# Optimization experiments

Measured on AMD Instinct MI355X. Metric: run time of the kernel, lower is better.

## Reference

```python
import jax, jax.numpy as jnp
import numpy as np

TEMPERATURE = 0.5
EPS = 1e-8  # torch F.cosine_similarity norm clamp


def setup_inputs() -> dict:
    key = jax.random.key(0)
    k1, k2 = jax.random.split(key)
    N, D = 4096, 256
    z1 = jax.random.normal(k1, (N, D), dtype=jnp.float32)
    z2 = jax.random.normal(k2, (N, D), dtype=jnp.float32)
    return {"z1": z1, "z2": z2}


def _l2norm(x):
    # matches torch cosine_similarity eps clamping on the norm
    n = jnp.sqrt(jnp.sum(x * x, axis=-1, keepdims=True))
    return x / jnp.maximum(n, EPS)


def reference(z1, z2):
    N = z1.shape[0]
    f = jnp.concatenate([z1, z2], axis=0)          # [2N, D]
    fn = _l2norm(f)                                 # row-normalized
    sim = fn @ fn.T                                 # [2N, 2N] cosine similarities
    diag = jnp.eye(2 * N, dtype=bool)
    # denominator: sum over off-diagonal entries (self-similarity excluded)
    denom = jnp.sum(jnp.where(diag, 0.0, jnp.exp(sim / TEMPERATURE)), axis=1)  # [2N]
    # positives: cosine(z1_i, z2_i), duplicated for both views
    z1n, z2n = _l2norm(z1), _l2norm(z2)
    pos = jnp.sum(z1n * z2n, axis=1)               # [N]
    pos = jnp.concatenate([pos, pos], axis=0)      # [2N]
    loss = -jnp.mean(jnp.log(jnp.exp(pos / TEMPERATURE) / denom))
    return loss
```

## Files before the change

### kernel.cpp

```cpp
#include <hip/hip_runtime.h>
#include <hip/hip_fp8.h>

#define D 256
#define SCALE 1.69864354f
#define EPS 1e-8f

typedef __attribute__((ext_vector_type(4))) float f32x4;
typedef long fp8x8;

__global__ __launch_bounds__(256) void normpos_kernel(
    const float* __restrict__ z1, const float* __restrict__ z2,
    unsigned char* __restrict__ fnq, float* __restrict__ pos,
    int* __restrict__ sync, int N) {
  if (blockIdx.x == 0 && threadIdx.x == 0) *sync = 0;
  int wid  = threadIdx.x >> 6;
  int lane = threadIdx.x & 63;
  int row  = blockIdx.x * 4 + wid;
  f32x4 a = *(const f32x4*)(z1 + (size_t)row * D + lane * 4);
  f32x4 b = *(const f32x4*)(z2 + (size_t)row * D + lane * 4);
  float s1  = a.x * a.x + a.y * a.y + a.z * a.z + a.w * a.w;
  float s2  = b.x * b.x + b.y * b.y + b.z * b.z + b.w * b.w;
  float dot = a.x * b.x + a.y * b.y + a.z * b.z + a.w * b.w;
  #pragma unroll
  for (int m = 1; m < 64; m <<= 1) {
    s1  += __shfl_xor(s1, m, 64);
    s2  += __shfl_xor(s2, m, 64);
    dot += __shfl_xor(dot, m, 64);
  }
  float inv1 = 1.0f / fmaxf(sqrtf(s1), EPS);
  float inv2 = 1.0f / fmaxf(sqrtf(s2), EPS);
  float q1 = inv1 * SCALE, q2 = inv2 * SCALE;
  unsigned int w1 = 0, w2 = 0;
  #pragma unroll
  for (int j = 0; j < 4; ++j) {
    w1 |= (unsigned int)__hip_cvt_float_to_fp8(a[j] * q1, __HIP_SATFINITE,
                                               __HIP_E4M3) << (8 * j);
    w2 |= (unsigned int)__hip_cvt_float_to_fp8(b[j] * q2, __HIP_SATFINITE,
                                               __HIP_E4M3) << (8 * j);
  }
  *(unsigned int*)(fnq + (size_t)row * D + lane * 4)       = w1;
  *(unsigned int*)(fnq + (size_t)(N + row) * D + lane * 4) = w2;
  if (lane == 0) pos[row] = dot * inv1 * inv2;
}


__device__ __forceinline__ void stage_tile(const unsigned char* __restrict__ row0,
                                           int kk, unsigned char* lds, int tid) {
  #pragma unroll
  for (int it = 0; it < 4; ++it) {
    int s = it * 256 + tid;
    int r = s >> 3;
    int p = s & 7;
    const unsigned char* src =
        row0 + (size_t)r * D + kk * 128 + ((p ^ (r & 7)) << 4);
    __builtin_amdgcn_global_load_lds(
        (const __attribute__((address_space(1))) void*)src,
        (__attribute__((address_space(3))) void*)(lds + s * 16), 16, 0, 0);
  }
}

__global__ __launch_bounds__(256, 4) void denom_kernel(
    const unsigned char* __restrict__ fnq, float* __restrict__ partial,
    int twoN) {
  __shared__ unsigned char As[128 * 128];
  __shared__ unsigned char Bs[128 * 128];

  int tid  = threadIdx.x;
  int wid  = tid >> 6;
  int lane = tid & 63;
  int c = lane & 15;
  int g = lane >> 4;
  int wr = wid >> 1, wc = wid & 1;

  int bid = blockIdx.x;
  int i = (int)((sqrtf(8.f * (float)bid + 1.f) - 1.f) * 0.5f);
  while ((i + 1) * (i + 2) / 2 <= bid) ++i;
  while (i * (i + 1) / 2 > bid) --i;
  int rb = bid - i * (i + 1) / 2;
  int cb = i;
  const unsigned char* Arow0 = fnq + (size_t)rb * 128 * D;
  const unsigned char* Brow0 = fnq + (size_t)cb * 128 * D;

  bool dblk  = (rb == cb);
  bool dwave = dblk && (wr == wc);

  f32x4 acc[4][4] = {};

  stage_tile(Arow0, 0, As, tid);
  stage_tile(Brow0, 0, Bs, tid);

  #pragma unroll
  for (int kk = 0; kk < 2; ++kk) {
    __syncthreads();
    #pragma unroll
    for (int ks = 0; ks < 4; ++ks) {
      fp8x8 a[4], b[4];
      int q  = (ks << 1) | (g >> 1);
      int h  = (g & 1) << 3;
      #pragma unroll
      for (int mi = 0; mi < 4; ++mi) {
        int ar = wr * 64 + mi * 16 + c;
        a[mi] = *(const fp8x8*)(As + ar * 128 + ((q ^ (ar & 7)) << 4) + h);
      }
      #pragma unroll
      for (int ni = 0; ni < 4; ++ni) {
        int bc = wc * 64 + ni * 16 + c;
        b[ni] = *(const fp8x8*)(Bs + bc * 128 + ((q ^ (bc & 7)) << 4) + h);
      }
      #pragma unroll
      for (int mi = 0; mi < 4; ++mi)
        #pragma unroll
        for (int ni = 0; ni < 4; ++ni)
          acc[mi][ni] = __builtin_amdgcn_mfma_f32_16x16x32_fp8_fp8(
              a[mi], b[ni], acc[mi][ni], 0, 0, 0);
    }
    if (kk == 0) {
      __syncthreads();
      stage_tile(Arow0, 1, As, tid);
      stage_tile(Brow0, 1, Bs, tid);
    }
  }

  float rsum[16];
  float csum[4];
  #pragma unroll
  for (int ii = 0; ii < 16; ++ii) rsum[ii] = 0.f;
  #pragma unroll
  for (int ii = 0; ii < 4; ++ii) csum[ii] = 0.f;

  if (dwave) {
    #pragma unroll
    for (int mi = 0; mi < 4; ++mi)
      #pragma unroll
      for (int ni = 0; ni < 4; ++ni) {
        int colloc = ni * 16 + c;
        #pragma unroll
        for (int r = 0; r < 4; ++r) {
          int rowloc = mi * 16 + g * 4 + r;
          float e = __builtin_amdgcn_exp2f(acc[mi][ni][r]);
          if (rowloc == colloc) e = 0.f;
          rsum[mi * 4 + r] += e;
        }
      }
  } else if (dblk) {
    #pragma unroll
    for (int mi = 0; mi < 4; ++mi)
      #pragma unroll
      for (int ni = 0; ni < 4; ++ni)
        #pragma unroll
        for (int r = 0; r < 4; ++r)
          rsum[mi * 4 + r] += __builtin_amdgcn_exp2f(acc[mi][ni][r]);
  } else {
    #pragma unroll
    for (int mi = 0; mi < 4; ++mi)
      #pragma unroll
      for (int ni = 0; ni < 4; ++ni)
        #pragma unroll
        for (int r = 0; r < 4; ++r) {
          float e = __builtin_amdgcn_exp2f(acc[mi][ni][r]);
          rsum[mi * 4 + r] += e;
          csum[ni]         += e;
        }
  }

  #pragma unroll
  for (int ii = 0; ii < 16; ++ii) {
    float v = rsum[ii];
    v += __shfl_xor(v, 1, 64);
    v += __shfl_xor(v, 2, 64);
    v += __shfl_xor(v, 4, 64);
    v += __shfl_xor(v, 8, 64);
    rsum[ii] = v;
  }
  if (!dblk) {
    #pragma unroll
    for (int ii = 0; ii < 4; ++ii) {
      float v = csum[ii];
      v += __shfl_xor(v, 16, 64);
      v += __shfl_xor(v, 32, 64);
      csum[ii] = v;
    }
  }

  __syncthreads();
  float* redR = (float*)As;
  float* redC = (float*)Bs;
  if (c == 0) {
    #pragma unroll
    for (int mi = 0; mi < 4; ++mi)
      #pragma unroll
      for (int r = 0; r < 4; ++r)
        redR[(wr * 64 + mi * 16 + g * 4 + r) * 2 + wc] = rsum[mi * 4 + r];
  }
  if (!dblk && g == 0) {
    #pragma unroll
    for (int ni = 0; ni < 4; ++ni)
      redC[(wc * 64 + ni * 16 + c) * 2 + wr] = csum[ni];
  }
  __syncthreads();
  if (tid < 128) {
    partial[(size_t)cb * twoN + rb * 128 + tid] =
        redR[tid * 2] + redR[tid * 2 + 1];
    if (rb != cb)
      partial[(size_t)rb * twoN + cb * 128 + tid] =
          redC[tid * 2] + redC[tid * 2 + 1];
  }
}

__global__ __launch_bounds__(256) void reduce_kernel(
    const float* __restrict__ partial, const float* __restrict__ pos,
    float* __restrict__ bsum, float* __restrict__ out, int* __restrict__ sync,
    int twoN, int N, int nsplit) {
  int row = blockIdx.x * 256 + threadIdx.x;
  int wid = threadIdx.x >> 6, lane = threadIdx.x & 63;
  float denom = 0.f;
  for (int s = 0; s < nsplit; ++s) denom += partial[(size_t)s * twoN + row];
  float ld = logf(denom);
  float p  = (row < N) ? pos[row] : 0.f;
  #pragma unroll
  for (int m = 1; m < 64; m <<= 1) {
    ld += __shfl_xor(ld, m, 64);
    p  += __shfl_xor(p, m, 64);
  }
  __shared__ float sld[4], spo[4];
  __shared__ int lastf;
  if (lane == 0) { sld[wid] = ld; spo[wid] = p; }
  __syncthreads();
  if (threadIdx.x == 0) {
    bsum[blockIdx.x]                = sld[0] + sld[1] + sld[2] + sld[3];
    bsum[gridDim.x + blockIdx.x]    = spo[0] + spo[1] + spo[2] + spo[3];
    __threadfence();
    lastf = (atomicAdd(sync, 1) == (int)gridDim.x - 1);
  }
  __syncthreads();
  if (lastf && threadIdx.x < 64) {
    __threadfence();
    int t = threadIdx.x;
    int nb = gridDim.x;
    float l2 = (t < nb) ? bsum[t] : 0.f;
    float p2 = (t < nb) ? bsum[nb + t] : 0.f;
    #pragma unroll
    for (int m = 1; m < 64; m <<= 1) {
      l2 += __shfl_xor(l2, m, 64);
      p2 += __shfl_xor(p2, m, 64);
    }
    if (t == 0) out[0] = l2 / (float)twoN - 2.f * (p2 / (float)N);
  }
}

extern "C" void kernel_launch(void* const* d_in, const int* in_sizes, int n_in,
                              void* d_out, int out_size, void* d_ws,
                              size_t ws_size, hipStream_t stream) {
  const float* z1 = (const float*)d_in[0];
  const float* z2 = (const float*)d_in[1];
  int N = in_sizes[0] / D;
  int twoN = 2 * N;
  int nrb = twoN / 128;

  unsigned char* fnq = (unsigned char*)d_ws;
  float* partial = (float*)((char*)d_ws + (size_t)twoN * D);
  float* pos     = (float*)((char*)partial + (size_t)nrb * twoN * 4);
  float* bsum    = (float*)((char*)pos + (size_t)N * 4);
  int*   sync    = (int*)((char*)bsum + 256 * 4);

  normpos_kernel<<<N / 4, 256, 0, stream>>>(z1, z2, fnq, pos, sync, N);
  int ntri = nrb * (nrb + 1) / 2;
  denom_kernel<<<ntri, 256, 0, stream>>>(fnq, partial, twoN);
  int nblk = twoN / 256;
  reduce_kernel<<<nblk, 256, 0, stream>>>(partial, pos, bsum, (float*)d_out,
                                          sync, twoN, N, nrb);
}
```

Measured before the change: 52.77 us.

## Stage full K=256 tiles in LDS once and reuse A tile on diagonal blocks

Replaces the two-step K staging with a single load of the full 128x256 fp8 A and B tiles into LDS, dropping the mid-loop barrier and restage. On diagonal blocks the B tile load is skipped and the A tile is reused as B. Separate reduction buffers remove the barrier needed before reusing the tile buffers. LDS use per block doubles to about 64KB and the min-blocks launch bound is removed, which lowers occupancy and removes the overlap of the second K stage with compute.

New measurement: 56.47 us. +7.0%, slower.

```diff
diff --git a/kernel.cpp b/kernel.cpp
--- a/kernel.cpp
+++ b/kernel.cpp
@@ -44,26 +44,13 @@
 }
 
 
-__device__ __forceinline__ void stage_tile(const unsigned char* __restrict__ row0,
-                                           int kk, unsigned char* lds, int tid) {
-  #pragma unroll
-  for (int it = 0; it < 4; ++it) {
-    int s = it * 256 + tid;
-    int r = s >> 3;
-    int p = s & 7;
-    const unsigned char* src =
-        row0 + (size_t)r * D + kk * 128 + ((p ^ (r & 7)) << 4);
-    __builtin_amdgcn_global_load_lds(
-        (const __attribute__((address_space(1))) void*)src,
-        (__attribute__((address_space(3))) void*)(lds + s * 16), 16, 0, 0);
-  }
-}
-
-__global__ __launch_bounds__(256, 4) void denom_kernel(
+__global__ __launch_bounds__(256) void denom_kernel(
     const unsigned char* __restrict__ fnq, float* __restrict__ partial,
     int twoN) {
-  __shared__ unsigned char As[128 * 128];
-  __shared__ unsigned char Bs[128 * 128];
+  __shared__ unsigned char As[128 * 256];
+  __shared__ unsigned char Bs[128 * 256];
+  __shared__ float redR[128][2];
+  __shared__ float redC[128][2];
 
   int tid  = threadIdx.x;
   int wid  = tid >> 6;
@@ -84,41 +71,56 @@
   bool dblk  = (rb == cb);
   bool dwave = dblk && (wr == wc);
 
+  #pragma unroll
+  for (int it = 0; it < 8; ++it) {
+    int s = it * 256 + tid;
+    int r = s >> 4;
+    int p = s & 15;
+    const unsigned char* src =
+        Arow0 + (size_t)r * D + ((p ^ (r & 7)) << 4);
+    __builtin_amdgcn_global_load_lds(
+        (const __attribute__((address_space(1))) void*)src,
+        (__attribute__((address_space(3))) void*)(As + s * 16), 16, 0, 0);
+  }
+  if (!dblk) {
+    #pragma unroll
+    for (int it = 0; it < 8; ++it) {
+      int s = it * 256 + tid;
+      int r = s >> 4;
+      int p = s & 15;
+      const unsigned char* src =
+          Brow0 + (size_t)r * D + ((p ^ (r & 7)) << 4);
+      __builtin_amdgcn_global_load_lds(
+          (const __attribute__((address_space(1))) void*)src,
+          (__attribute__((address_space(3))) void*)(Bs + s * 16), 16, 0, 0);
+    }
+  }
+  __syncthreads();
+
+  const unsigned char* Bbase = dblk ? As : Bs;
+
   f32x4 acc[4][4] = {};
-
-  stage_tile(Arow0, 0, As, tid);
-  stage_tile(Brow0, 0, Bs, tid);
-
-  #pragma unroll
-  for (int kk = 0; kk < 2; ++kk) {
-    __syncthreads();
-    #pragma unroll
-    for (int ks = 0; ks < 4; ++ks) {
-      fp8x8 a[4], b[4];
-      int q  = (ks << 1) | (g >> 1);
-      int h  = (g & 1) << 3;
-      #pragma unroll
-      for (int mi = 0; mi < 4; ++mi) {
-        int ar = wr * 64 + mi * 16 + c;
-        a[mi] = *(const fp8x8*)(As + ar * 128 + ((q ^ (ar & 7)) << 4) + h);
-      }
-      #pragma unroll
-      for (int ni = 0; ni < 4; ++ni) {
-        int bc = wc * 64 + ni * 16 + c;
-        b[ni] = *(const fp8x8*)(Bs + bc * 128 + ((q ^ (bc & 7)) << 4) + h);
-      }
-      #pragma unroll
-      for (int mi = 0; mi < 4; ++mi)
-        #pragma unroll
-        for (int ni = 0; ni < 4; ++ni)
-          acc[mi][ni] = __builtin_amdgcn_mfma_f32_16x16x32_fp8_fp8(
-              a[mi], b[ni], acc[mi][ni], 0, 0, 0);
-    }
-    if (kk == 0) {
-      __syncthreads();
-      stage_tile(Arow0, 1, As, tid);
-      stage_tile(Brow0, 1, Bs, tid);
-    }
+  #pragma unroll
+  for (int ks = 0; ks < 8; ++ks) {
+    fp8x8 a[4], b[4];
+    int q = (ks << 1) | (g >> 1);
+    int h = (g & 1) << 3;
+    #pragma unroll
+    for (int mi = 0; mi < 4; ++mi) {
+      int ar = wr * 64 + mi * 16 + c;
+      a[mi] = *(const fp8x8*)(As + ar * 256 + ((q ^ (ar & 7)) << 4) + h);
+    }
+    #pragma unroll
+    for (int ni = 0; ni < 4; ++ni) {
+      int bc = wc * 64 + ni * 16 + c;
+      b[ni] = *(const fp8x8*)(Bbase + bc * 256 + ((q ^ (bc & 7)) << 4) + h);
+    }
+    #pragma unroll
+    for (int mi = 0; mi < 4; ++mi)
+      #pragma unroll
+      for (int ni = 0; ni < 4; ++ni)
+        acc[mi][ni] = __builtin_amdgcn_mfma_f32_16x16x32_fp8_fp8(
+            a[mi], b[ni], acc[mi][ni], 0, 0, 0);
   }
 
   float rsum[16];
@@ -172,6 +174,13 @@
     v += __shfl_xor(v, 8, 64);
     rsum[ii] = v;
   }
+  if (c == 0) {
+    #pragma unroll
+    for (int mi = 0; mi < 4; ++mi)
+      #pragma unroll
+      for (int r = 0; r < 4; ++r)
+        redR[wr * 64 + mi * 16 + g * 4 + r][wc] = rsum[mi * 4 + r];
+  }
   if (!dblk) {
     #pragma unroll
     for (int ii = 0; ii < 4; ++ii) {
@@ -180,30 +189,19 @@
       v += __shfl_xor(v, 32, 64);
       csum[ii] = v;
     }
-  }
-
-  __syncthreads();
-  float* redR = (float*)As;
-  float* redC = (float*)Bs;
-  if (c == 0) {
-    #pragma unroll
-    for (int mi = 0; mi < 4; ++mi)
-      #pragma unroll
-      for (int r = 0; r < 4; ++r)
-        redR[(wr * 64 + mi * 16 + g * 4 + r) * 2 + wc] = rsum[mi * 4 + r];
-  }
-  if (!dblk && g == 0) {
-    #pragma unroll
-    for (int ni = 0; ni < 4; ++ni)
-      redC[(wc * 64 + ni * 16 + c) * 2 + wr] = csum[ni];
+    if (g == 0) {
+      #pragma unroll
+      for (int ni = 0; ni < 4; ++ni)
+        redC[wc * 64 + ni * 16 + c][wr] = csum[ni];
+    }
   }
   __syncthreads();
   if (tid < 128) {
     partial[(size_t)cb * twoN + rb * 128 + tid] =
-        redR[tid * 2] + redR[tid * 2 + 1];
+        redR[tid][0] + redR[tid][1];
     if (rb != cb)
       partial[(size_t)rb * twoN + cb * 128 + tid] =
-          redC[tid * 2] + redC[tid * 2 + 1];
+          redC[tid][0] + redC[tid][1];
   }
 }
 
@@ -227,8 +225,8 @@
   if (lane == 0) { sld[wid] = ld; spo[wid] = p; }
   __syncthreads();
   if (threadIdx.x == 0) {
-    bsum[blockIdx.x]                = sld[0] + sld[1] + sld[2] + sld[3];
-    bsum[gridDim.x + blockIdx.x]    = spo[0] + spo[1] + spo[2] + spo[3];
+    bsum[blockIdx.x]             = sld[0] + sld[1] + sld[2] + sld[3];
+    bsum[gridDim.x + blockIdx.x] = spo[0] + spo[1] + spo[2] + spo[3];
     __threadfence();
     lastf = (atomicAdd(sync, 1) == (int)gridDim.x - 1);
   }
```
